# Kernel tuning notes

Measured on AMD Instinct MI355X. Metric: run time of the kernel, lower is better.

Reference implementation:

```python
import jax, jax.numpy as jnp
import numpy as np

N = 100000
E = 1250000
D = 64
K = 3
A_COEF = 1.0
B_COEF = 1.0
L_DOM = -1.0
R_DOM = 1.0


def setup_inputs() -> dict:
    key = jax.random.key(0)
    k1, k2, k3, k4, k5 = jax.random.split(key, 5)
    x = jax.random.normal(k1, (N, D), dtype=jnp.float32)
    edge_index = jax.random.randint(k2, (2, E), 0, N, dtype=jnp.int64)
    edge_weight = jax.random.uniform(k3, (E,), dtype=jnp.float32)
    alpha_params = jnp.ones((K + 1,), dtype=jnp.float32)
    lin_w = jax.random.normal(k4, ((K + 1) * D, D), dtype=jnp.float32) / np.sqrt((K + 1) * D)
    lin_b = jnp.zeros((D,), dtype=jnp.float32)
    return {"x": x, "edge_index": edge_index, "edge_weight": edge_weight,
            "alpha_params": alpha_params, "lin_w": lin_w, "lin_b": lin_b}


def reference(x, edge_index, edge_weight, alpha_params, lin_w, lin_b):
    row, col = edge_index[0], edge_index[1]
    # gcn normalization: deg from source nodes, deg<0.5 -> +1
    deg = jax.ops.segment_sum(jnp.ones((E,), x.dtype), row, num_segments=N)
    deg = jnp.where(deg < 0.5, deg + 1.0, deg)
    dis = deg ** -0.5
    val = dis[row] * edge_weight * dis[col]  # [E]

    def spmm(h):  # adj @ h : out[row] += val * h[col]
        return jax.ops.segment_sum(val[:, None] * h[col], row, num_segments=N)

    alphas = jnp.tanh(alpha_params)  # basealpha = 1.0
    a, b, l, r = A_COEF, B_COEF, L_DOM, R_DOM
    xs = [x]
    for L in range(1, K + 1):
        Ax = spmm(xs[-1])
        if L == 1:
            coef1 = (a - b) / 2 - (a + b + 2) / 2 * ((l + r) / (r - l))
            coef2 = (a + b + 2) / (r - l)
            nxt = alphas[0] * (coef1 * xs[-1] + coef2 * Ax)
        else:
            coef_l = 2 * L * (L + a + b) * (2 * L - 2 + a + b)
            coef_lm1_1 = (2 * L + a + b - 1) * (2 * L + a + b) * (2 * L + a + b - 2)
            coef_lm1_2 = (2 * L + a + b - 1) * (a ** 2 - b ** 2)
            coef_lm2 = 2 * (L - 1 + a) * (L - 1 + b) * (2 * L + a + b)
            tmp1 = alphas[L - 1] * (coef_lm1_1 / coef_l)
            tmp2 = alphas[L - 1] * (coef_lm1_2 / coef_l)
            tmp3 = alphas[L - 1] * alphas[L - 2] * (coef_lm2 / coef_l)
            tmp1_2 = tmp1 * (2.0 / (r - l))
            tmp2_2 = tmp1 * ((r + l) / (r - l)) + tmp2
            nxt = tmp1_2 * Ax - tmp2_2 * xs[-1] - tmp3 * xs[-2]
        xs.append(nxt)
    x_cat = jnp.concatenate(xs, axis=1)  # [N, (K+1)*D]
    return x_cat @ lin_w + lin_b
```

## Files before the change

### kernel.cpp

```cpp
#include <hip/hip_runtime.h>
#include <hip/hip_bf16.h>
#include <math.h>

#define NN 100000
#define EE 1250000
#define DD 64

typedef __attribute__((ext_vector_type(8))) short short8;
typedef __attribute__((ext_vector_type(8))) unsigned short u16x8;
typedef __attribute__((ext_vector_type(4))) float f32x4;

__device__ __forceinline__ unsigned short f2b(float f) {
    unsigned u = __float_as_uint(f);
    u += 0x7fffu + ((u >> 16) & 1u);
    return (unsigned short)(u >> 16);
}
__device__ __forceinline__ float b2f(unsigned short h) {
    return __uint_as_float(((unsigned)h) << 16);
}

__global__ __launch_bounds__(256) void scan_a(const int* __restrict__ degi,
                                              int* __restrict__ rowStart,
                                              int* __restrict__ bs, int N) {
    __shared__ int s[256];
    int tid = threadIdx.x;
    int i = blockIdx.x * 256 + tid;
    int v = (i < N) ? degi[i] : 0;
    s[tid] = v;
    __syncthreads();
    for (int off = 1; off < 256; off <<= 1) {
        int t = (tid >= off) ? s[tid - off] : 0;
        __syncthreads();
        s[tid] += t;
        __syncthreads();
    }
    if (i < N) rowStart[i] = s[tid] - v;
    if (tid == 255) bs[blockIdx.x] = s[255];
}

__global__ __launch_bounds__(512) void scan_b(int* __restrict__ bs, int nb) {
    __shared__ int s[512];
    int tid = threadIdx.x;
    int v = (tid < nb) ? bs[tid] : 0;
    s[tid] = v;
    __syncthreads();
    for (int off = 1; off < 512; off <<= 1) {
        int t = (tid >= off) ? s[tid - off] : 0;
        __syncthreads();
        s[tid] += t;
        __syncthreads();
    }
    if (tid < nb) bs[tid] = s[tid] - v;
}

__global__ __launch_bounds__(256) void scan_c(int* __restrict__ rowStart,
                                              const int* __restrict__ bs,
                                              int N, int E) {
    int i = blockIdx.x * 256 + threadIdx.x;
    if (i < N) rowStart[i] += bs[blockIdx.x];
    if (i == 0) rowStart[N] = E;
}

__global__ __launch_bounds__(256) void dis_kernel(const int* __restrict__ degi,
                                                  float* __restrict__ dis, int N) {
    int i = blockIdx.x * 256 + threadIdx.x;
    if (i >= N) return;
    int d = degi[i];
    float df = (d == 0) ? 1.0f : (float)d;
    dis[i] = 1.0f / sqrtf(df);
}

#define NSL 125
#define SLR 800
#define NSEG 16
#define SEGCAP 768
#define CPAD 16
#define VSCL (1.0f / 32768.0f)
__global__ __launch_bounds__(256) void binA(const int* __restrict__ row,
                                            const int* __restrict__ col,
                                            const float* __restrict__ w,
                                            uint2* __restrict__ sbuf,
                                            int* __restrict__ segCnt, int E4) {
    __shared__ int cnt[NSL];
    __shared__ int base[NSL];
    int tid = threadIdx.x;
    if (tid < NSL) cnt[tid] = 0;
    __syncthreads();
    int g = blockIdx.x & (NSEG - 1);
    int i4 = blockIdx.x * 256 + tid;
    bool act = (i4 < E4);
    int4 r4, c4;
    float4 w4;
    int sl[4], loc[4], rk[4];
    unsigned evp[4];
    if (act) {
        r4 = ((const int4*)row)[i4];
        c4 = ((const int4*)col)[i4];
        w4 = ((const float4*)w)[i4];
        int rr[4] = {r4.x, r4.y, r4.z, r4.w};
        int cc[4] = {c4.x, c4.y, c4.z, c4.w};
        float ww[4] = {w4.x, w4.y, w4.z, w4.w};
        #pragma unroll
        for (int k = 0; k < 4; ++k) {
            int r = rr[k], c = cc[k];
            int wq = (int)(ww[k] * 32768.0f + 0.5f);
            wq = (wq > 32767) ? 32767 : wq;
            evp[k] = ((unsigned)c << 15) | (unsigned)wq;
            rk[k] = r;
            sl[k] = r / SLR;
            loc[k] = atomicAdd(&cnt[sl[k]], 1);
        }
    }
    __syncthreads();
    if (tid < NSL) {
        int c = cnt[tid];
        if (c) base[tid] = atomicAdd(&segCnt[(tid * NSEG + g) * CPAD], c);
    }
    __syncthreads();
    if (act) {
        #pragma unroll
        for (int k = 0; k < 4; ++k) {
            int p = base[sl[k]] + loc[k];
            if (p < SEGCAP)
                sbuf[(size_t)(sl[k] * NSEG + g) * SEGCAP + p] =
                    make_uint2(evp[k], (unsigned)rk[k]);
        }
    }
}

__global__ __launch_bounds__(512) void deg_slice(const uint2* __restrict__ sbuf,
                                                 const int* __restrict__ segCnt,
                                                 int* __restrict__ degi) {
    __shared__ int dcnt[SLR];
    __shared__ int scnt[NSEG];
    int tid = threadIdx.x;
    int s = blockIdx.x;
    int r0 = s * SLR;
    for (int i = tid; i < SLR; i += 512) dcnt[i] = 0;
    if (tid < NSEG) {
        int c = segCnt[(s * NSEG + tid) * CPAD];
        scnt[tid] = (c > SEGCAP) ? SEGCAP : c;
    }
    __syncthreads();
    for (int slot = tid * 4; slot < NSEG * SEGCAP; slot += 2048) {
        int g = slot / SEGCAP;
        int off = slot - g * SEGCAP;
        int cg = scnt[g];
        if (off >= cg) continue;
        const uint2* seg = sbuf + (size_t)(s * NSEG + g) * SEGCAP;
        uint4 a = *(const uint4*)(seg + off);
        uint4 b = *(const uint4*)(seg + off + 2);
        atomicAdd(&dcnt[(int)a.y - r0], 1);
        if (off + 1 < cg) atomicAdd(&dcnt[(int)a.w - r0], 1);
        if (off + 2 < cg) atomicAdd(&dcnt[(int)b.y - r0], 1);
        if (off + 3 < cg) atomicAdd(&dcnt[(int)b.w - r0], 1);
    }
    __syncthreads();
    for (int i = tid; i < SLR; i += 512) {
        int gr = r0 + i;
        if (gr < NN) degi[gr] = dcnt[i];
    }
}

__global__ __launch_bounds__(512) void binB(const uint2* __restrict__ sbuf,
                                            const int* __restrict__ segCnt,
                                            const int* __restrict__ rowStart,
                                            const float* __restrict__ dis,
                                            unsigned* __restrict__ ev) {
    __shared__ int curs[SLR];
    __shared__ int rs[SLR];
    __shared__ float dsl[SLR];
    __shared__ int scnt[NSEG];
    int tid = threadIdx.x;
    int s = blockIdx.x;
    int r0 = s * SLR;
    for (int i = tid; i < SLR; i += 512) {
        curs[i] = 0;
        int gr = r0 + i;
        rs[i] = (gr < NN) ? rowStart[gr] : 0;
        dsl[i] = (gr < NN) ? dis[gr] : 1.0f;
    }
    if (tid < NSEG) {
        int c = segCnt[(s * NSEG + tid) * CPAD];
        scnt[tid] = (c > SEGCAP) ? SEGCAP : c;
    }
    __syncthreads();
    for (int slot = tid * 4; slot < NSEG * SEGCAP; slot += 2048) {
        int g = slot / SEGCAP;
        int off = slot - g * SEGCAP;
        int cg = scnt[g];
        if (off >= cg) continue;
        const uint2* seg = sbuf + (size_t)(s * NSEG + g) * SEGCAP;
        uint4 a = *(const uint4*)(seg + off);
        uint4 b = *(const uint4*)(seg + off + 2);
        unsigned pk[4] = {a.x, a.z, b.x, b.z};
        unsigned rr[4] = {a.y, a.w, b.y, b.w};
        int nv = cg - off;
        nv = (nv > 4) ? 4 : nv;
        #pragma unroll 4
        for (int k = 0; k < 4; ++k) {
            if (k >= nv) break;
            int rl = (int)rr[k] - r0;
            int c = (int)(pk[k] >> 15);
            float wv = (float)(pk[k] & 0x7fffu) * VSCL;
            float v = dsl[rl] * wv * dis[c];
            int vq = (int)(v * 32768.0f + 0.5f);
            vq = (vq > 32767) ? 32767 : vq;
            ev[rs[rl] + atomicAdd(&curs[rl], 1)] = ((unsigned)c << 15) | (unsigned)vq;
        }
    }
}

__global__ void coef_kernel(const float* __restrict__ ap, float* __restrict__ coef) {
    if (threadIdx.x != 0 || blockIdx.x != 0) return;
    const float a = 1.0f, b = 1.0f, l = -1.0f, r = 1.0f;
    float als[3];
    als[0] = tanhf(ap[0]);
    als[1] = tanhf(ap[1]);
    als[2] = tanhf(ap[2]);
    float coef1 = (a - b) * 0.5f - (a + b + 2.0f) * 0.5f * ((l + r) / (r - l));
    float coef2 = (a + b + 2.0f) / (r - l);
    coef[0] = als[0] * coef1;
    coef[1] = als[0] * coef2;
    for (int L = 2; L <= 3; ++L) {
        float Lf = (float)L;
        float coef_l     = 2.0f * Lf * (Lf + a + b) * (2.0f * Lf - 2.0f + a + b);
        float coef_lm1_1 = (2.0f * Lf + a + b - 1.0f) * (2.0f * Lf + a + b) * (2.0f * Lf + a + b - 2.0f);
        float coef_lm1_2 = (2.0f * Lf + a + b - 1.0f) * (a * a - b * b);
        float coef_lm2   = 2.0f * (Lf - 1.0f + a) * (Lf - 1.0f + b) * (2.0f * Lf + a + b);
        float tmp1   = als[L - 1] * (coef_lm1_1 / coef_l);
        float tmp2   = als[L - 1] * (coef_lm1_2 / coef_l);
        float tmp3   = als[L - 1] * als[L - 2] * (coef_lm2 / coef_l);
        float tmp1_2 = tmp1 * (2.0f / (r - l));
        float tmp2_2 = tmp1 * ((r + l) / (r - l)) + tmp2;
        int base = 2 + (L - 2) * 3;
        coef[base + 0] = tmp1_2;
        coef[base + 1] = tmp2_2;
        coef[base + 2] = tmp3;
    }
}

__global__ __launch_bounds__(256) void tobf16(const float4* __restrict__ in,
                                              ushort4* __restrict__ outb, int n4) {
    int i = blockIdx.x * 256 + threadIdx.x;
    if (i >= n4) return;
    float4 v = in[i];
    ushort4 o;
    o.x = f2b(v.x); o.y = f2b(v.y); o.z = f2b(v.z); o.w = f2b(v.w);
    outb[i] = o;
}

__global__ __launch_bounds__(256) void wt_kernel(const float* __restrict__ W,
                                                 unsigned short* __restrict__ Wt) {
    int idx = blockIdx.x * 256 + threadIdx.x;
    int n = idx >> 8, k = idx & 255;
    Wt[idx] = f2b(W[k * 64 + n]);
}

__device__ __forceinline__ void fma8(float* a, unsigned u, u16x8 h) {
    float v = (float)(u & 0x7fffu) * VSCL;
    #pragma unroll
    for (int c = 0; c < 8; ++c) a[c] += v * b2f(h[c]);
}

template <int MODE>
__global__ __launch_bounds__(256) void spmm_fused(const int* __restrict__ rowStart,
                                                  const unsigned* __restrict__ ev,
                                                  const unsigned short* __restrict__ hb,
                                                  const unsigned short* __restrict__ xm1,
                                                  const unsigned short* __restrict__ xm2,
                                                  unsigned short* __restrict__ outb,
                                                  const float* __restrict__ coef,
                                                  int cbase, int N) {
    int t = blockIdx.x * 256 + threadIdx.x;
    int r = t >> 3;
    if (r >= N) return;
    int q = t & 7;
    int s0 = rowStart[r];
    int s1 = rowStart[r + 1];
    float a[8];
    #pragma unroll
    for (int c = 0; c < 8; ++c) a[c] = 0.f;
    int j = s0;
    for (; j + 3 < s1; j += 4) {
        unsigned u0 = ev[j];
        unsigned u1 = ev[j + 1];
        unsigned u2 = ev[j + 2];
        unsigned u3 = ev[j + 3];
        u16x8 h0 = *(const u16x8*)&hb[(size_t)(u0 >> 15) * 64 + q * 8];
        u16x8 h1 = *(const u16x8*)&hb[(size_t)(u1 >> 15) * 64 + q * 8];
        u16x8 h2 = *(const u16x8*)&hb[(size_t)(u2 >> 15) * 64 + q * 8];
        u16x8 h3 = *(const u16x8*)&hb[(size_t)(u3 >> 15) * 64 + q * 8];
        fma8(a, u0, h0);
        fma8(a, u1, h1);
        fma8(a, u2, h2);
        fma8(a, u3, h3);
    }
    for (; j < s1; ++j) {
        unsigned u0 = ev[j];
        u16x8 h0 = *(const u16x8*)&hb[(size_t)(u0 >> 15) * 64 + q * 8];
        fma8(a, u0, h0);
    }
    size_t oi = (size_t)r * 64 + q * 8;
    float o[8];
    if (MODE == 0) {
        float c0 = coef[cbase], c1 = coef[cbase + 1];
        u16x8 m1 = *(const u16x8*)&xm1[oi];
        #pragma unroll
        for (int c = 0; c < 8; ++c) o[c] = c0 * b2f(m1[c]) + c1 * a[c];
    } else {
        float c0 = coef[cbase], c1 = coef[cbase + 1], c2 = coef[cbase + 2];
        u16x8 m1 = *(const u16x8*)&xm1[oi];
        u16x8 m2 = *(const u16x8*)&xm2[oi];
        #pragma unroll
        for (int c = 0; c < 8; ++c)
            o[c] = c0 * a[c] - c1 * b2f(m1[c]) - c2 * b2f(m2[c]);
    }
    u16x8 ob;
    #pragma unroll
    for (int c = 0; c < 8; ++c) ob[c] = f2b(o[c]);
    *(u16x8*)&outb[oi] = ob;
}

__global__ __launch_bounds__(256, 4) void final_gemm_mfma(
        const ushort4* __restrict__ x0,
        const ushort4* __restrict__ x1,
        const ushort4* __restrict__ x2,
        const ushort4* __restrict__ x3,
        const unsigned short* __restrict__ Wt,
        const float* __restrict__ bias,
        float* __restrict__ out) {
    const int tid = threadIdx.x;
    const int lane = tid & 63;
    const int w = tid >> 6;
    const int m = lane & 15;
    const int quad = lane >> 4;
    const int n0 = (int)blockIdx.x * 128;

    int gr0 = n0 + 16 * w + m;
    int gr1 = gr0 + 64;
    size_t ar0 = (size_t)((gr0 < NN) ? gr0 : 0) * 16;
    size_t ar1 = (size_t)((gr1 < NN) ? gr1 : 0) * 16;

    f32x4 acc0[4], acc1[4];
    #pragma unroll
    for (int nt = 0; nt < 4; ++nt) {
        acc0[nt] = (f32x4){0.f, 0.f, 0.f, 0.f};
        acc1[nt] = (f32x4){0.f, 0.f, 0.f, 0.f};
    }

    #pragma unroll
    for (int ks = 0; ks < 8; ++ks) {
        const ushort4* p = (ks < 2) ? x0 : (ks < 4) ? x1 : (ks < 6) ? x2 : x3;
        size_t ko = (size_t)((ks & 1) * 8 + quad * 2);
        short8 af0 = *(const short8*)&p[ar0 + ko];
        short8 af1 = *(const short8*)&p[ar1 + ko];
        #pragma unroll
        for (int nt = 0; nt < 4; ++nt) {
            short8 bf = *(const short8*)&Wt[(nt * 16 + m) * 256 + ks * 32 + quad * 8];
            acc0[nt] = __builtin_amdgcn_mfma_f32_16x16x32_bf16(af0, bf, acc0[nt], 0, 0, 0);
            acc1[nt] = __builtin_amdgcn_mfma_f32_16x16x32_bf16(af1, bf, acc1[nt], 0, 0, 0);
        }
    }

    #pragma unroll
    for (int nt = 0; nt < 4; ++nt) {
        float bv = bias[nt * 16 + m];
        #pragma unroll
        for (int rg = 0; rg < 4; ++rg) {
            int node0 = n0 + 16 * w + quad * 4 + rg;
            int node1 = node0 + 64;
            if (node0 < NN) out[(size_t)node0 * 64 + nt * 16 + m] = acc0[nt][rg] + bv;
            if (node1 < NN) out[(size_t)node1 * 64 + nt * 16 + m] = acc1[nt][rg] + bv;
        }
    }
}

extern "C" void kernel_launch(void* const* d_in, const int* in_sizes, int n_in,
                              void* d_out, int out_size, void* d_ws, size_t ws_size,
                              hipStream_t stream) {
    const float* x  = (const float*)d_in[0];
    const int*   ei = (const int*)d_in[1];
    const float* ew = (const float*)d_in[2];
    const float* ap = (const float*)d_in[3];
    const float* lw = (const float*)d_in[4];
    const float* lb = (const float*)d_in[5];
    float* out = (float*)d_out;

    const int N = NN, E = EE;
    const int ND = N * DD;

    const int* row = ei;
    const int* col = ei + E;

    char* ws = (char*)d_ws;
    ushort4* xb = (ushort4*)ws;
    ushort4* Ab = (ushort4*)(ws + (size_t)ND * 2);
    ushort4* Bb = (ushort4*)(ws + (size_t)ND * 4);
    ushort4* Cb = (ushort4*)(ws + (size_t)ND * 6);
    uint2*   sbuf   = (uint2*)(ws + (size_t)ND * 4);
    int*     segCnt = (int*)(ws + (size_t)ND * 6);
    unsigned* ev = (unsigned*)(ws + (size_t)ND * 8);
    char* sm    = ws + (size_t)ND * 8 + (size_t)E * 4;
    float* coef     = (float*)sm;
    float* dis      = (float*)(sm + 256);
    int*   degi     = (int*)(sm + 256 + (size_t)N * 4);
    int*   rowStart = (int*)(sm + 256 + (size_t)N * 8);
    int*   bs       = (int*)(sm + 256 + (size_t)N * 12 + 64);
    unsigned short* Wt = (unsigned short*)(sm + 256 + (size_t)N * 12 + 64 + 4096);

    const int gridN  = (N + 255) / 256;
    const int gridSp = (N * 8) / 256;
    const int gridCv = (ND / 4) / 256;
    const int gridG  = (N + 127) / 128;
    const int E4     = E / 4;
    const int gridA  = (E4 + 255) / 256;

    hipMemsetAsync(segCnt, 0, (size_t)NSL * NSEG * CPAD * 4, stream);
    coef_kernel<<<1, 64, 0, stream>>>(ap, coef);
    wt_kernel<<<64, 256, 0, stream>>>(lw, Wt);
    binA<<<gridA, 256, 0, stream>>>(row, col, ew, sbuf, segCnt, E4);
    deg_slice<<<NSL, 512, 0, stream>>>(sbuf, segCnt, degi);
    scan_a<<<gridN, 256, 0, stream>>>(degi, rowStart, bs, N);
    scan_b<<<1, 512, 0, stream>>>(bs, gridN);
    scan_c<<<gridN, 256, 0, stream>>>(rowStart, bs, N, E);
    dis_kernel<<<gridN, 256, 0, stream>>>(degi, dis, N);
    binB<<<NSL, 512, 0, stream>>>(sbuf, segCnt, rowStart, dis, ev);

    tobf16<<<gridCv, 256, 0, stream>>>((const float4*)x, xb, ND / 4);

    spmm_fused<0><<<gridSp, 256, 0, stream>>>(rowStart, ev,
                                              (const unsigned short*)xb,
                                              (const unsigned short*)xb,
                                              (const unsigned short*)xb,
                                              (unsigned short*)Ab, coef, 0, N);
    spmm_fused<1><<<gridSp, 256, 0, stream>>>(rowStart, ev,
                                              (const unsigned short*)Ab,
                                              (const unsigned short*)Ab,
                                              (const unsigned short*)xb,
                                              (unsigned short*)Bb, coef, 2, N);
    spmm_fused<1><<<gridSp, 256, 0, stream>>>(rowStart, ev,
                                              (const unsigned short*)Bb,
                                              (const unsigned short*)Bb,
                                              (const unsigned short*)Ab,
                                              (unsigned short*)Cb, coef, 5, N);

    final_gemm_mfma<<<gridG, 256, 0, stream>>>(xb, Ab, Bb, Cb, Wt, lb, out);
}
```

Measured before the change: 251.9 us.

## Merge small setup kernels, fuse dis into scan, unroll SpMM by 8 with nontemporal loads

Folds the segCnt memset, coefficient computation and weight transpose into one kernel, and computes dis inside scan_a, cutting four launches. The SpMM inner loop gains an 8-way unrolled path that issues more independent gathers per thread. Edge stream, residual reads and output stores now use nontemporal hints so they do not evict the gathered feature rows from cache. The wider unroll raises register pressure, and the hints could hurt if the outputs are reread soon after by the next SpMM.

```diff
diff --git a/kernel.cpp b/kernel.cpp
--- a/kernel.cpp
+++ b/kernel.cpp
@@ -21,7 +21,8 @@
 
 __global__ __launch_bounds__(256) void scan_a(const int* __restrict__ degi,
                                               int* __restrict__ rowStart,
-                                              int* __restrict__ bs, int N) {
+                                              int* __restrict__ bs,
+                                              float* __restrict__ dis, int N) {
     __shared__ int s[256];
     int tid = threadIdx.x;
     int i = blockIdx.x * 256 + tid;
@@ -34,7 +35,11 @@
         s[tid] += t;
         __syncthreads();
     }
-    if (i < N) rowStart[i] = s[tid] - v;
+    if (i < N) {
+        rowStart[i] = s[tid] - v;
+        float df = (v == 0) ? 1.0f : (float)v;
+        dis[i] = 1.0f / sqrtf(df);
+    }
     if (tid == 255) bs[blockIdx.x] = s[255];
 }
 
@@ -59,15 +64,6 @@
     int i = blockIdx.x * 256 + threadIdx.x;
     if (i < N) rowStart[i] += bs[blockIdx.x];
     if (i == 0) rowStart[N] = E;
-}
-
-__global__ __launch_bounds__(256) void dis_kernel(const int* __restrict__ degi,
-                                                  float* __restrict__ dis, int N) {
-    int i = blockIdx.x * 256 + threadIdx.x;
-    if (i >= N) return;
-    int d = degi[i];
-    float df = (d == 0) ? 1.0f : (float)d;
-    dis[i] = 1.0f / sqrtf(df);
 }
 
 #define NSL 125
@@ -211,32 +207,41 @@
     }
 }
 
-__global__ void coef_kernel(const float* __restrict__ ap, float* __restrict__ coef) {
-    if (threadIdx.x != 0 || blockIdx.x != 0) return;
-    const float a = 1.0f, b = 1.0f, l = -1.0f, r = 1.0f;
-    float als[3];
-    als[0] = tanhf(ap[0]);
-    als[1] = tanhf(ap[1]);
-    als[2] = tanhf(ap[2]);
-    float coef1 = (a - b) * 0.5f - (a + b + 2.0f) * 0.5f * ((l + r) / (r - l));
-    float coef2 = (a + b + 2.0f) / (r - l);
-    coef[0] = als[0] * coef1;
-    coef[1] = als[0] * coef2;
-    for (int L = 2; L <= 3; ++L) {
-        float Lf = (float)L;
-        float coef_l     = 2.0f * Lf * (Lf + a + b) * (2.0f * Lf - 2.0f + a + b);
-        float coef_lm1_1 = (2.0f * Lf + a + b - 1.0f) * (2.0f * Lf + a + b) * (2.0f * Lf + a + b - 2.0f);
-        float coef_lm1_2 = (2.0f * Lf + a + b - 1.0f) * (a * a - b * b);
-        float coef_lm2   = 2.0f * (Lf - 1.0f + a) * (Lf - 1.0f + b) * (2.0f * Lf + a + b);
-        float tmp1   = als[L - 1] * (coef_lm1_1 / coef_l);
-        float tmp2   = als[L - 1] * (coef_lm1_2 / coef_l);
-        float tmp3   = als[L - 1] * als[L - 2] * (coef_lm2 / coef_l);
-        float tmp1_2 = tmp1 * (2.0f / (r - l));
-        float tmp2_2 = tmp1 * ((r + l) / (r - l)) + tmp2;
-        int base = 2 + (L - 2) * 3;
-        coef[base + 0] = tmp1_2;
-        coef[base + 1] = tmp2_2;
-        coef[base + 2] = tmp3;
+__global__ __launch_bounds__(256) void wt_coef(const float* __restrict__ W,
+                                               unsigned short* __restrict__ Wt,
+                                               const float* __restrict__ ap,
+                                               float* __restrict__ coef,
+                                               int* __restrict__ segCnt) {
+    int idx = blockIdx.x * 256 + threadIdx.x;
+    int n = idx >> 8, k = idx & 255;
+    Wt[idx] = f2b(W[k * 64 + n]);
+    for (int z = idx; z < NSL * NSEG * CPAD; z += 16384) segCnt[z] = 0;
+    if (idx == 0) {
+        const float a = 1.0f, b = 1.0f, l = -1.0f, r = 1.0f;
+        float als[3];
+        als[0] = tanhf(ap[0]);
+        als[1] = tanhf(ap[1]);
+        als[2] = tanhf(ap[2]);
+        float coef1 = (a - b) * 0.5f - (a + b + 2.0f) * 0.5f * ((l + r) / (r - l));
+        float coef2 = (a + b + 2.0f) / (r - l);
+        coef[0] = als[0] * coef1;
+        coef[1] = als[0] * coef2;
+        for (int L = 2; L <= 3; ++L) {
+            float Lf = (float)L;
+            float coef_l     = 2.0f * Lf * (Lf + a + b) * (2.0f * Lf - 2.0f + a + b);
+            float coef_lm1_1 = (2.0f * Lf + a + b - 1.0f) * (2.0f * Lf + a + b) * (2.0f * Lf + a + b - 2.0f);
+            float coef_lm1_2 = (2.0f * Lf + a + b - 1.0f) * (a * a - b * b);
+            float coef_lm2   = 2.0f * (Lf - 1.0f + a) * (Lf - 1.0f + b) * (2.0f * Lf + a + b);
+            float tmp1   = als[L - 1] * (coef_lm1_1 / coef_l);
+            float tmp2   = als[L - 1] * (coef_lm1_2 / coef_l);
+            float tmp3   = als[L - 1] * als[L - 2] * (coef_lm2 / coef_l);
+            float tmp1_2 = tmp1 * (2.0f / (r - l));
+            float tmp2_2 = tmp1 * ((r + l) / (r - l)) + tmp2;
+            int base = 2 + (L - 2) * 3;
+            coef[base + 0] = tmp1_2;
+            coef[base + 1] = tmp2_2;
+            coef[base + 2] = tmp3;
+        }
     }
 }
 
@@ -248,13 +253,6 @@
     ushort4 o;
     o.x = f2b(v.x); o.y = f2b(v.y); o.z = f2b(v.z); o.w = f2b(v.w);
     outb[i] = o;
-}
-
-__global__ __launch_bounds__(256) void wt_kernel(const float* __restrict__ W,
-                                                 unsigned short* __restrict__ Wt) {
-    int idx = blockIdx.x * 256 + threadIdx.x;
-    int n = idx >> 8, k = idx & 255;
-    Wt[idx] = f2b(W[k * 64 + n]);
 }
 
 __device__ __forceinline__ void fma8(float* a, unsigned u, u16x8 h) {
@@ -282,11 +280,22 @@
     #pragma unroll
     for (int c = 0; c < 8; ++c) a[c] = 0.f;
     int j = s0;
+    for (; j + 7 < s1; j += 8) {
+        unsigned u[8];
+        u16x8 h[8];
+        #pragma unroll
+        for (int k = 0; k < 8; ++k) u[k] = __builtin_nontemporal_load(&ev[j + k]);
+        #pragma unroll
+        for (int k = 0; k < 8; ++k)
+            h[k] = *(const u16x8*)&hb[(size_t)(u[k] >> 15) * 64 + q * 8];
+        #pragma unroll
+        for (int k = 0; k < 8; ++k) fma8(a, u[k], h[k]);
+    }
     for (; j + 3 < s1; j += 4) {
-        unsigned u0 = ev[j];
-        unsigned u1 = ev[j + 1];
-        unsigned u2 = ev[j + 2];
-        unsigned u3 = ev[j + 3];
+        unsigned u0 = __builtin_nontemporal_load(&ev[j]);
+        unsigned u1 = __builtin_nontemporal_load(&ev[j + 1]);
+        unsigned u2 = __builtin_nontemporal_load(&ev[j + 2]);
+        unsigned u3 = __builtin_nontemporal_load(&ev[j + 3]);
         u16x8 h0 = *(const u16x8*)&hb[(size_t)(u0 >> 15) * 64 + q * 8];
         u16x8 h1 = *(const u16x8*)&hb[(size_t)(u1 >> 15) * 64 + q * 8];
         u16x8 h2 = *(const u16x8*)&hb[(size_t)(u2 >> 15) * 64 + q * 8];
@@ -297,7 +306,7 @@
         fma8(a, u3, h3);
     }
     for (; j < s1; ++j) {
-        unsigned u0 = ev[j];
+        unsigned u0 = __builtin_nontemporal_load(&ev[j]);
         u16x8 h0 = *(const u16x8*)&hb[(size_t)(u0 >> 15) * 64 + q * 8];
         fma8(a, u0, h0);
     }
@@ -305,13 +314,13 @@
     float o[8];
     if (MODE == 0) {
         float c0 = coef[cbase], c1 = coef[cbase + 1];
-        u16x8 m1 = *(const u16x8*)&xm1[oi];
+        u16x8 m1 = __builtin_nontemporal_load((const u16x8*)&xm1[oi]);
         #pragma unroll
         for (int c = 0; c < 8; ++c) o[c] = c0 * b2f(m1[c]) + c1 * a[c];
     } else {
         float c0 = coef[cbase], c1 = coef[cbase + 1], c2 = coef[cbase + 2];
-        u16x8 m1 = *(const u16x8*)&xm1[oi];
-        u16x8 m2 = *(const u16x8*)&xm2[oi];
+        u16x8 m1 = __builtin_nontemporal_load((const u16x8*)&xm1[oi]);
+        u16x8 m2 = __builtin_nontemporal_load((const u16x8*)&xm2[oi]);
         #pragma unroll
         for (int c = 0; c < 8; ++c)
             o[c] = c0 * a[c] - c1 * b2f(m1[c]) - c2 * b2f(m2[c]);
@@ -319,7 +328,7 @@
     u16x8 ob;
     #pragma unroll
     for (int c = 0; c < 8; ++c) ob[c] = f2b(o[c]);
-    *(u16x8*)&outb[oi] = ob;
+    __builtin_nontemporal_store(ob, (u16x8*)&outb[oi]);
 }
 
 __global__ __launch_bounds__(256, 4) void final_gemm_mfma(
@@ -416,15 +425,12 @@
     const int E4     = E / 4;
     const int gridA  = (E4 + 255) / 256;
 
-    hipMemsetAsync(segCnt, 0, (size_t)NSL * NSEG * CPAD * 4, stream);
-    coef_kernel<<<1, 64, 0, stream>>>(ap, coef);
-    wt_kernel<<<64, 256, 0, stream>>>(lw, Wt);
+    wt_coef<<<64, 256, 0, stream>>>(lw, Wt, ap, coef, segCnt);
     binA<<<gridA, 256, 0, stream>>>(row, col, ew, sbuf, segCnt, E4);
     deg_slice<<<NSL, 512, 0, stream>>>(sbuf, segCnt, degi);
-    scan_a<<<gridN, 256, 0, stream>>>(degi, rowStart, bs, N);
+    scan_a<<<gridN, 256, 0, stream>>>(degi, rowStart, bs, dis, N);
     scan_b<<<1, 512, 0, stream>>>(bs, gridN);
     scan_c<<<gridN, 256, 0, stream>>>(rowStart, bs, N, E);
-    dis_kernel<<<gridN, 256, 0, stream>>>(degi, dis, N);
     binB<<<NSL, 512, 0, stream>>>(sbuf, segCnt, rowStart, dis, ev);
 
     tobf16<<<gridCv, 256, 0, stream>>>((const float4*)x, xb, ND / 4);
```

Result: slower. 265.5 us (+5.4%).
